# Kernel tuning notes

Hardware: AMD Instinct MI355X
Metric: run time of the kernel (lower is better)

The kernel has to match this reference:

```python
import jax, jax.numpy as jnp
import numpy as np

HEAD_DIM = 32
KSIZE = 3
SCALE = HEAD_DIM ** (-0.5)  # self.scale = head_dim ** -0.5 with head_dim=32


def setup_inputs() -> dict:
    key = jax.random.key(0)
    kq, kk, kv = jax.random.split(key, 3)
    shape = (4, 128, 128, 128)  # (B, d, H, W)
    return {
        "q": jax.random.normal(kq, shape, dtype=jnp.float32),
        "k": jax.random.normal(kk, shape, dtype=jnp.float32),
        "v": jax.random.normal(kv, shape, dtype=jnp.float32),
    }


def _unfold3(x):
    # nn.Unfold(kernel_size=3, dilation=1, padding=1, stride=1):
    # [B, d, H, W] -> [B, d, 9, H, W], kernel positions in row-major (ki, kj)
    B, d, H, W = x.shape
    xp = jnp.pad(x, ((0, 0), (0, 0), (1, 1), (1, 1)))
    return jnp.stack(
        [xp[:, :, i:i + H, j:j + W] for i in range(KSIZE) for j in range(KSIZE)],
        axis=2,
    )


def reference(q, k, v):
    B, d, H, W = q.shape
    h = d // HEAD_DIM  # number of heads
    n = H * W
    # q: [B, h, head_dim, n]
    qh = q.reshape(B, h, HEAD_DIM, n)
    # k patches: [B, h, head_dim, 9, n]
    kp = _unfold3(k).reshape(B, h, HEAD_DIM, KSIZE * KSIZE, n)
    # attn: [B, h, n, 9] = (q . k_neighbor) * scale, softmax over the 9 neighbors
    attn = jnp.einsum('bhcn,bhckn->bhnk', qh, kp) * SCALE
    attn = jax.nn.softmax(attn, axis=-1)
    # v patches: [B, h, head_dim, 9, n]
    vp = _unfold3(v).reshape(B, h, HEAD_DIM, KSIZE * KSIZE, n)
    # out: [B, n, h, head_dim] -> [B, H, W, d] (head-major channel layout, as in torch)
    out = jnp.einsum('bhnk,bhckn->bnhc', attn, vp).reshape(B, H, W, d)
    return jax.nn.relu(out)
```

## Files before the change

kernel.cpp:

```cpp
#include <hip/hip_runtime.h>
#include <stdint.h>

#define HW 128
#define PLANE (HW * HW)
#define SCALE 0.17677669529663687f
#define FENCE() asm volatile("" ::: "memory")
#define VMW(N) asm volatile("s_waitcnt vmcnt(" #N ")" ::: "memory")
#define BAR() __builtin_amdgcn_s_barrier()

__device__ __forceinline__ void dma16(const float* g, float* l) {
  __builtin_amdgcn_global_load_lds(
      (const __attribute__((address_space(1))) void*)g,
      (__attribute__((address_space(3))) void*)l, 16, 0, 0);
}

__global__ __launch_bounds__(512, 2) void natt3x3_kernel(
    const float* __restrict__ q,
    const float* __restrict__ k,
    const float* __restrict__ v,
    float* __restrict__ out) {
  __shared__ __align__(16) float smem[3 * 10240];

  const int tid  = threadIdx.x;
  const int lane = tid & 63;
  const int w    = tid >> 6;
  const int h2   = lane & 1;
  const int s    = lane >> 1;
  const int x0   = s << 2;
  const int bid  = blockIdx.x;
  const int img   = ((bid & 7) << 1) | ((bid >> 3) & 1);
  const int ytile = bid >> 4;
  const int head  = img & 3;
  const int b     = img >> 2;
  const int y0    = ytile << 3;
  const int y     = y0 + w;

  const size_t ibase = (size_t)(b * 128 + head * 32) * PLANE;
  const size_t cbase = ibase + (size_t)(h2 * 4) * PLANE;
  const int yx = y * HW + x0;

  const int hi  = lane >> 5;
  const int spx = (lane & 31) << 2;
  int srow[5];
#pragma unroll
  for (int j = 0; j < 5; ++j) {
    int rg = y0 - 1 + 2 * j + hi;
    rg = rg < 0 ? 0 : (rg > HW - 1 ? HW - 1 : rg);
    srow[j] = rg * HW + spx;
  }
  float* const dwave = smem + w * 1280;

  float l[4][9];
#pragma unroll
  for (int i = 0; i < 4; ++i)
#pragma unroll
    for (int j = 0; j < 9; ++j) l[i][j] = 0.f;
  float acc[4][16];
#pragma unroll
  for (int i = 0; i < 4; ++i)
#pragma unroll
    for (int c = 0; c < 16; ++c) acc[i][c] = 0.f;
  float4 qA[4], qB[4];

#define DMA(BUF, PTR, G) do {                                                 \
    const float* sb = (PTR) + ibase + (size_t)((G) * 8 + w) * PLANE;          \
    float* db = dwave + (BUF) * 10240;                                        \
    _Pragma("unroll")                                                         \
    for (int j = 0; j < 5; ++j) dma16(sb + srow[j], db + j * 256);            \
  } while (0)

#define LQ(QW, G) do {                                                        \
    const float* qg = q + cbase + (size_t)((G) * 8) * PLANE + yx;             \
    _Pragma("unroll")                                                         \
    for (int c = 0; c < 4; ++c)                                               \
      QW[c] = *reinterpret_cast<const float4*>(qg + (size_t)c * PLANE);       \
  } while (0)

#define SKV(BUF, C, DY)                                                       \
  (*reinterpret_cast<const float4*>(                                          \
      smem + (BUF) * 10240 + (h2 * 4 + (C)) * 1280 + (w + (DY)) * 128 + x0))

#define CQK(BUF, QW) do {                                                     \
    _Pragma("unroll")                                                         \
    for (int c = 0; c < 4; ++c) {                                             \
      const float qa[4] = {QW[c].x * SCALE, QW[c].y * SCALE,                  \
                           QW[c].z * SCALE, QW[c].w * SCALE};                 \
      _Pragma("unroll")                                                       \
      for (int dy = 0; dy < 3; ++dy) {                                        \
        float4 kq = SKV(BUF, c, dy);                                          \
        float n0 = __shfl_up(kq.w, 2);                                        \
        float n5 = __shfl_down(kq.x, 2);                                      \
        const float n[6] = {n0, kq.x, kq.y, kq.z, kq.w, n5};                  \
        _Pragma("unroll")                                                     \
        for (int i = 0; i < 4; ++i)                                           \
          _Pragma("unroll")                                                   \
          for (int j = 0; j < 3; ++j)                                         \
            l[i][dy * 3 + j] += qa[i] * n[i + j];                             \
      }                                                                       \
    }                                                                         \
  } while (0)

#define CPV(BUF, G) do {                                                      \
    _Pragma("unroll")                                                         \
    for (int c = 0; c < 4; ++c)                                               \
      _Pragma("unroll")                                                       \
      for (int dy = 0; dy < 3; ++dy) {                                        \
        float4 vq = SKV(BUF, c, dy);                                          \
        float n0 = __shfl_up(vq.w, 2);                                        \
        float n5 = __shfl_down(vq.x, 2);                                      \
        const float n[6] = {n0, vq.x, vq.y, vq.z, vq.w, n5};                  \
        _Pragma("unroll")                                                     \
        for (int i = 0; i < 4; ++i)                                           \
          _Pragma("unroll")                                                   \
          for (int j = 0; j < 3; ++j)                                         \
            acc[i][(G) * 4 + c] += l[i][dy * 3 + j] * n[i + j];               \
      }                                                                       \
  } while (0)

  LQ(qA, 0);     FENCE();
  DMA(0, k, 0);  FENCE();
  DMA(1, k, 1);  FENCE();
  LQ(qB, 1);     FENCE();
  DMA(2, k, 2);  FENCE();
  VMW(14); BAR(); FENCE();
  CQK(0, qA);    FENCE(); BAR(); FENCE();
  LQ(qA, 2);     FENCE();
  DMA(0, k, 3);  FENCE();
  VMW(18); BAR(); FENCE();
  CQK(1, qB);    FENCE(); BAR(); FENCE();
  LQ(qB, 3);     FENCE();
  DMA(1, v, 0);  FENCE();
  VMW(18); BAR(); FENCE();
  CQK(2, qA);    FENCE(); BAR(); FENCE();
  DMA(2, v, 1);  FENCE();
  VMW(14); BAR(); FENCE();
  CQK(0, qB);    FENCE();

#pragma unroll
  for (int i = 0; i < 4; ++i)
#pragma unroll
    for (int j = 0; j < 9; ++j) l[i][j] += __shfl_xor(l[i][j], 1);
#pragma unroll
  for (int i = 0; i < 4; ++i) {
    const int xp = x0 + i;
    float mk[9];
#pragma unroll
    for (int dy = 0; dy < 3; ++dy)
#pragma unroll
      for (int dx = 0; dx < 3; ++dx) {
        bool ok = ((unsigned)(y + dy - 1) < (unsigned)HW) &&
                  ((unsigned)(xp + dx - 1) < (unsigned)HW);
        mk[dy * 3 + dx] = ok ? 1.f : 0.f;
      }
    float m = -1e30f;
#pragma unroll
    for (int j = 0; j < 9; ++j) {
      float t = l[i][j] * mk[j];
      l[i][j] = t;
      m = fmaxf(m, t);
    }
    float sum = 0.f;
#pragma unroll
    for (int j = 0; j < 9; ++j) {
      float e = __expf(l[i][j] - m);
      l[i][j] = e;
      sum += e;
    }
    float inv = 1.f / sum;
#pragma unroll
    for (int j = 0; j < 9; ++j) l[i][j] *= inv * mk[j];
  }
  FENCE(); BAR(); FENCE();
  DMA(0, v, 2);  FENCE();
  VMW(10); BAR(); FENCE();
  CPV(1, 0);     FENCE(); BAR(); FENCE();
  DMA(1, v, 3);  FENCE();
  VMW(10); BAR(); FENCE();
  CPV(2, 1);     FENCE(); BAR(); FENCE();
  VMW(5); BAR(); FENCE();
  CPV(0, 2);     FENCE(); BAR(); FENCE();
  VMW(0); BAR(); FENCE();
  CPV(1, 3);

  const size_t obase = ((size_t)(b * PLANE + y * HW)) * 128 + head * 32 + h2 * 4;
#pragma unroll
  for (int i = 0; i < 4; ++i) {
    float* op = out + obase + (size_t)(x0 + i) * 128;
#pragma unroll
    for (int g = 0; g < 4; ++g) {
      float4 o;
      o.x = fmaxf(acc[i][g * 4 + 0], 0.f);
      o.y = fmaxf(acc[i][g * 4 + 1], 0.f);
      o.z = fmaxf(acc[i][g * 4 + 2], 0.f);
      o.w = fmaxf(acc[i][g * 4 + 3], 0.f);
      *reinterpret_cast<float4*>(op + g * 8) = o;
    }
  }

#undef DMA
#undef LQ
#undef SKV
#undef CQK
#undef CPV
}

extern "C" void kernel_launch(void* const* d_in, const int* in_sizes, int n_in,
                              void* d_out, int out_size, void* d_ws, size_t ws_size,
                              hipStream_t stream) {
  const float* q = (const float*)d_in[0];
  const float* k = (const float*)d_in[1];
  const float* v = (const float*)d_in[2];
  float* out = (float*)d_out;
  natt3x3_kernel<<<256, 512, 0, stream>>>(q, k, v, out);
}
```

Measured before the change: 31.83 us.

## Switch to two large double-buffered stages of 16 channels with early stores

Replaces the triple-buffered 8-channel K/V staging with double-buffered 16-channel stages, halving the number of barrier phases. Each wave now issues DMA for two channel planes, and the first half of the output is stored before the last V stage is processed. LDS usage doubles to 160KB, so launch bounds drop to one block per CU and inter-block overlap is lost.

```diff
diff --git a/kernel.cpp b/kernel.cpp
--- a/kernel.cpp
+++ b/kernel.cpp
@@ -14,12 +14,12 @@
       (__attribute__((address_space(3))) void*)l, 16, 0, 0);
 }
 
-__global__ __launch_bounds__(512, 2) void natt3x3_kernel(
+__global__ __launch_bounds__(512, 1) void natt3x3_kernel(
     const float* __restrict__ q,
     const float* __restrict__ k,
     const float* __restrict__ v,
     float* __restrict__ out) {
-  __shared__ __align__(16) float smem[3 * 10240];
+  __shared__ __align__(16) float smem[2 * 20480];
 
   const int tid  = threadIdx.x;
   const int lane = tid & 63;
@@ -48,7 +48,6 @@
     rg = rg < 0 ? 0 : (rg > HW - 1 ? HW - 1 : rg);
     srow[j] = rg * HW + spx;
   }
-  float* const dwave = smem + w * 1280;
 
   float l[4][9];
 #pragma unroll
@@ -60,13 +59,16 @@
   for (int i = 0; i < 4; ++i)
 #pragma unroll
     for (int c = 0; c < 16; ++c) acc[i][c] = 0.f;
-  float4 qA[4], qB[4];
-
-#define DMA(BUF, PTR, G) do {                                                 \
-    const float* sb = (PTR) + ibase + (size_t)((G) * 8 + w) * PLANE;          \
-    float* db = dwave + (BUF) * 10240;                                        \
-    _Pragma("unroll")                                                         \
-    for (int j = 0; j < 5; ++j) dma16(sb + srow[j], db + j * 256);            \
+  float4 qv0[4], qv1[4], qv2[4], qv3[4];
+
+#define DMA(BUF, PTR, CB) do {                                                \
+    const float* sb0 = (PTR) + ibase + (size_t)((CB) + 2 * w) * PLANE;        \
+    const float* sb1 = sb0 + PLANE;                                           \
+    float* db = smem + (BUF) * 20480 + (2 * w) * 1280;                        \
+    _Pragma("unroll")                                                         \
+    for (int j = 0; j < 5; ++j) dma16(sb0 + srow[j], db + j * 256);           \
+    _Pragma("unroll")                                                         \
+    for (int j = 0; j < 5; ++j) dma16(sb1 + srow[j], db + 1280 + j * 256);    \
   } while (0)
 
 #define LQ(QW, G) do {                                                        \
@@ -76,18 +78,18 @@
       QW[c] = *reinterpret_cast<const float4*>(qg + (size_t)c * PLANE);       \
   } while (0)
 
-#define SKV(BUF, C, DY)                                                       \
+#define SKV(BUF, CL, DY)                                                      \
   (*reinterpret_cast<const float4*>(                                          \
-      smem + (BUF) * 10240 + (h2 * 4 + (C)) * 1280 + (w + (DY)) * 128 + x0))
-
-#define CQK(BUF, QW) do {                                                     \
+      smem + (BUF) * 20480 + (CL) * 1280 + (w + (DY)) * 128 + x0))
+
+#define CQK1(BUF, QW, GL) do {                                                \
     _Pragma("unroll")                                                         \
     for (int c = 0; c < 4; ++c) {                                             \
       const float qa[4] = {QW[c].x * SCALE, QW[c].y * SCALE,                  \
                            QW[c].z * SCALE, QW[c].w * SCALE};                 \
       _Pragma("unroll")                                                       \
       for (int dy = 0; dy < 3; ++dy) {                                        \
-        float4 kq = SKV(BUF, c, dy);                                          \
+        float4 kq = SKV(BUF, (GL) * 8 + h2 * 4 + c, dy);                      \
         float n0 = __shfl_up(kq.w, 2);                                        \
         float n5 = __shfl_down(kq.x, 2);                                      \
         const float n[6] = {n0, kq.x, kq.y, kq.z, kq.w, n5};                  \
@@ -100,12 +102,12 @@
     }                                                                         \
   } while (0)
 
-#define CPV(BUF, G) do {                                                      \
+#define CPV1(BUF, GL, GO) do {                                                \
     _Pragma("unroll")                                                         \
     for (int c = 0; c < 4; ++c)                                               \
       _Pragma("unroll")                                                       \
       for (int dy = 0; dy < 3; ++dy) {                                        \
-        float4 vq = SKV(BUF, c, dy);                                          \
+        float4 vq = SKV(BUF, (GL) * 8 + h2 * 4 + c, dy);                      \
         float n0 = __shfl_up(vq.w, 2);                                        \
         float n5 = __shfl_down(vq.x, 2);                                      \
         const float n[6] = {n0, vq.x, vq.y, vq.z, vq.w, n5};                  \
@@ -113,28 +115,42 @@
         for (int i = 0; i < 4; ++i)                                           \
           _Pragma("unroll")                                                   \
           for (int j = 0; j < 3; ++j)                                         \
-            acc[i][(G) * 4 + c] += l[i][dy * 3 + j] * n[i + j];               \
+            acc[i][(GO) * 4 + c] += l[i][dy * 3 + j] * n[i + j];              \
       }                                                                       \
   } while (0)
 
-  LQ(qA, 0);     FENCE();
-  DMA(0, k, 0);  FENCE();
-  DMA(1, k, 1);  FENCE();
-  LQ(qB, 1);     FENCE();
-  DMA(2, k, 2);  FENCE();
-  VMW(14); BAR(); FENCE();
-  CQK(0, qA);    FENCE(); BAR(); FENCE();
-  LQ(qA, 2);     FENCE();
-  DMA(0, k, 3);  FENCE();
-  VMW(18); BAR(); FENCE();
-  CQK(1, qB);    FENCE(); BAR(); FENCE();
-  LQ(qB, 3);     FENCE();
-  DMA(1, v, 0);  FENCE();
-  VMW(18); BAR(); FENCE();
-  CQK(2, qA);    FENCE(); BAR(); FENCE();
-  DMA(2, v, 1);  FENCE();
-  VMW(14); BAR(); FENCE();
-  CQK(0, qB);    FENCE();
+  const size_t obase = ((size_t)(b * PLANE + y * HW)) * 128 + head * 32 + h2 * 4;
+#define ST(P) do {                                                            \
+    _Pragma("unroll")                                                         \
+    for (int i = 0; i < 4; ++i) {                                             \
+      float* op = out + obase + (size_t)(x0 + i) * 128 + (P) * 16;            \
+      float4 o;                                                               \
+      o.x = fmaxf(acc[i][(P) * 8 + 0], 0.f);                                  \
+      o.y = fmaxf(acc[i][(P) * 8 + 1], 0.f);                                  \
+      o.z = fmaxf(acc[i][(P) * 8 + 2], 0.f);                                  \
+      o.w = fmaxf(acc[i][(P) * 8 + 3], 0.f);                                  \
+      *reinterpret_cast<float4*>(op) = o;                                     \
+      o.x = fmaxf(acc[i][(P) * 8 + 4], 0.f);                                  \
+      o.y = fmaxf(acc[i][(P) * 8 + 5], 0.f);                                  \
+      o.z = fmaxf(acc[i][(P) * 8 + 6], 0.f);                                  \
+      o.w = fmaxf(acc[i][(P) * 8 + 7], 0.f);                                  \
+      *reinterpret_cast<float4*>(op + 8) = o;                                 \
+    }                                                                         \
+  } while (0)
+
+  LQ(qv0, 0);   FENCE();
+  LQ(qv1, 1);   FENCE();
+  DMA(0, k, 0); FENCE();
+  VMW(0); BAR(); FENCE();
+
+  DMA(1, k, 16); FENCE();
+  LQ(qv2, 2);    FENCE();
+  LQ(qv3, 3);    FENCE();
+  CQK1(0, qv0, 0); CQK1(0, qv1, 1); FENCE();
+  VMW(8); BAR(); FENCE();
+
+  DMA(0, v, 0); FENCE();
+  CQK1(1, qv2, 0); CQK1(1, qv3, 1); FENCE();
 
 #pragma unroll
   for (int i = 0; i < 4; ++i)
@@ -170,38 +186,23 @@
 #pragma unroll
     for (int j = 0; j < 9; ++j) l[i][j] *= inv * mk[j];
   }
-  FENCE(); BAR(); FENCE();
-  DMA(0, v, 2);  FENCE();
-  VMW(10); BAR(); FENCE();
-  CPV(1, 0);     FENCE(); BAR(); FENCE();
-  DMA(1, v, 3);  FENCE();
-  VMW(10); BAR(); FENCE();
-  CPV(2, 1);     FENCE(); BAR(); FENCE();
-  VMW(5); BAR(); FENCE();
-  CPV(0, 2);     FENCE(); BAR(); FENCE();
+  FENCE();
   VMW(0); BAR(); FENCE();
-  CPV(1, 3);
-
-  const size_t obase = ((size_t)(b * PLANE + y * HW)) * 128 + head * 32 + h2 * 4;
-#pragma unroll
-  for (int i = 0; i < 4; ++i) {
-    float* op = out + obase + (size_t)(x0 + i) * 128;
-#pragma unroll
-    for (int g = 0; g < 4; ++g) {
-      float4 o;
-      o.x = fmaxf(acc[i][g * 4 + 0], 0.f);
-      o.y = fmaxf(acc[i][g * 4 + 1], 0.f);
-      o.z = fmaxf(acc[i][g * 4 + 2], 0.f);
-      o.w = fmaxf(acc[i][g * 4 + 3], 0.f);
-      *reinterpret_cast<float4*>(op + g * 8) = o;
-    }
-  }
+
+  DMA(1, v, 16); FENCE();
+  CPV1(0, 0, 0); CPV1(0, 1, 1); FENCE();
+  ST(0); FENCE();
+  VMW(8); BAR(); FENCE();
+
+  CPV1(1, 0, 2); CPV1(1, 1, 3); FENCE();
+  ST(1);
 
 #undef DMA
 #undef LQ
 #undef SKV
-#undef CQK
-#undef CPV
+#undef CQK1
+#undef CPV1
+#undef ST
 }
 
 extern "C" void kernel_launch(void* const* d_in, const int* in_sizes, int n_in,
```

Measured after the change: 30.85 us. 3.1% less time.
